# Kernel tuning notes

Hardware: AMD Instinct MI355X
Metric: run time of the kernel (lower is better)

Reference implementation:

```python
import jax, jax.numpy as jnp
import numpy as np

B, SQ, SE, H, NH = 2, 2048, 2048, 1024, 16
HD = H // NH  # 64

def setup_inputs() -> dict:
    key = jax.random.key(0)
    ks = jax.random.split(key, 8)
    s = 1.0 / np.sqrt(H)
    return {
        "hidden_states": jax.random.normal(ks[0], (B, SQ, H), jnp.float32),
        "encoder_hidden_states": jax.random.normal(ks[1], (B, SE, H), jnp.float32),
        "attention_mask": jnp.zeros((B, 1, 1, SQ + SE), jnp.float32),
        "Wq": jax.random.normal(ks[2], (H, H), jnp.float32) * s,
        "bq": jnp.zeros((H,), jnp.float32),
        "Wk": jax.random.normal(ks[3], (H, H), jnp.float32) * s,
        "bk": jnp.zeros((H,), jnp.float32),
        "Wv": jax.random.normal(ks[4], (H, H), jnp.float32) * s,
        "bv": jnp.zeros((H,), jnp.float32),
    }

def _split_heads(x):
    # [B, S, H] -> [B, NH, S, HD]
    b, s, _ = x.shape
    return x.reshape(b, s, NH, HD).transpose(0, 2, 1, 3)

def reference(hidden_states, encoder_hidden_states, attention_mask, Wq, bq, Wk, bk, Wv, bv):
    # Q from self tokens; K,V from concat(self, encoder) along sequence
    all_hs = jnp.concatenate([hidden_states, encoder_hidden_states], axis=1)  # [B, SQ+SE, H]
    q = _split_heads(hidden_states @ Wq + bq)   # [B, NH, SQ, HD]
    k = _split_heads(all_hs @ Wk + bk)          # [B, NH, SKV, HD]
    v = _split_heads(all_hs @ Wv + bv)          # [B, NH, SKV, HD]
    scores = jnp.einsum('bhqd,bhkd->bhqk', q, k) / jnp.sqrt(jnp.float32(HD))
    scores = scores + attention_mask            # additive mask, broadcast [B,1,1,SKV]
    probs = jax.nn.softmax(scores, axis=-1)     # dropout p=0 (eval)
    ctx = jnp.einsum('bhqk,bhkd->bhqd', probs, v)
    ctx = ctx.transpose(0, 2, 1, 3).reshape(hidden_states.shape[0], hidden_states.shape[1], H)
    return ctx
```

## Files before the change

### kernel.cpp

```cpp
#include <hip/hip_runtime.h>
#include <hip/hip_bf16.h>
#include <stdint.h>


typedef __attribute__((ext_vector_type(8))) short short8;
typedef __attribute__((ext_vector_type(4))) float f32x4;
typedef __attribute__((ext_vector_type(16))) float f32x16;
typedef __attribute__((ext_vector_type(4))) unsigned short us4;
typedef __attribute__((ext_vector_type(4))) unsigned int u32x4;

typedef __attribute__((ext_vector_type(8), may_alias)) short short8a;
typedef __attribute__((ext_vector_type(4), may_alias)) float f32x4a;
typedef __attribute__((may_alias)) float floata;

#define DEV static __device__ __forceinline__

DEV unsigned short f2bf(float f) {
  unsigned int u = __builtin_bit_cast(unsigned int, f);
  u += 0x7fffu + ((u >> 16) & 1u);
  return (unsigned short)(u >> 16);
}

DEV float exp2_(float x) {
#if __has_builtin(__builtin_amdgcn_exp2f)
  return __builtin_amdgcn_exp2f(x);
#else
  float r; asm("v_exp_f32 %0, %1" : "=v"(r) : "v"(x)); return r;
#endif
}

DEV unsigned int cvtpk_bf16(float lo, float hi) {
  unsigned int r;
  asm("v_cvt_pk_bf16_f32 %0, %1, %2" : "=v"(r) : "v"(lo), "v"(hi));
  return r;
}

DEV void g2lds16(const void* g, void* l) {
  __builtin_amdgcn_global_load_lds((const __attribute__((address_space(1))) void*)g,
                                   (__attribute__((address_space(3))) void*)l, 16, 0, 0);
}

__global__ __launch_bounds__(256) void convert_allhs(const float* __restrict__ hid,
                                                     const float* __restrict__ enc,
                                                     unsigned short* __restrict__ ah) {
  int idx = blockIdx.x * 256 + threadIdx.x;
  const int perB = 4096 * 256;
  int b = idx / perB, r = idx - b * perB;
  int s = r >> 8, c4 = r & 255;
  const float* srcrow = (s < 2048) ? hid + (size_t)(b * 2048 + s) * 1024
                                   : enc + (size_t)(b * 2048 + (s - 2048)) * 1024;
  f32x4 v = *(const f32x4*)(srcrow + c4 * 4);
  us4 o;
  o[0] = f2bf(v[0]); o[1] = f2bf(v[1]); o[2] = f2bf(v[2]); o[3] = f2bf(v[3]);
  *(us4*)(ah + (size_t)idx * 4) = o;
}

__global__ __launch_bounds__(256) void premul_mask(const float* __restrict__ m,
                                                   float* __restrict__ o) {
  int i = blockIdx.x * 256 + threadIdx.x;
  o[i] = m[i] * 1.4426950408889634f;
}

__global__ __launch_bounds__(256) void transpose_w3(const float* __restrict__ Wq,
                                                    const float* __restrict__ Wk,
                                                    const float* __restrict__ Wv,
                                                    unsigned short* __restrict__ WtBase) {
  __shared__ unsigned short t[64][65];
  const int z = blockIdx.z;
  const float* W = (z == 0) ? Wq : (z == 1) ? Wk : Wv;
  unsigned short* Wt = WtBase + (size_t)z * 1048576;
  int k0 = blockIdx.y * 64, n0 = blockIdx.x * 64;
  int tid = threadIdx.x;
#pragma unroll
  for (int rep = 0; rep < 16; rep++) {
    int idx = rep * 256 + tid;
    int kk = idx >> 6, nn = idx & 63;
    t[kk][nn] = f2bf(W[(size_t)(k0 + kk) * 1024 + n0 + nn]);
  }
  __syncthreads();
#pragma unroll
  for (int rep = 0; rep < 16; rep++) {
    int idx = rep * 256 + tid;
    int nn = idx >> 6, kk = idx & 63;
    Wt[(size_t)(n0 + nn) * 1024 + k0 + kk] = t[kk][nn];
  }
}

__global__ __launch_bounds__(256) void gemm_all(const unsigned short* __restrict__ WTQ,
                                                const unsigned short* __restrict__ WTK,
                                                const unsigned short* __restrict__ WTV,
                                                const unsigned short* __restrict__ AH,
                                                const float* __restrict__ bq,
                                                const float* __restrict__ bk,
                                                const float* __restrict__ bv,
                                                unsigned short* __restrict__ Qout,
                                                unsigned short* __restrict__ Kout,
                                                unsigned short* __restrict__ Vout,
                                                float qscale) {
  __shared__ unsigned short ldsA[128 * 32];
  __shared__ unsigned short ldsB[128 * 32];

  int id = blockIdx.x;
  int f2 = (id & 7) * 160 + (id >> 3);

  const unsigned short *A, *Bm;
  const float* bias;
  unsigned short* outb;
  int S, mode, r0, c0;
  float osc = 1.0f;
  if (f2 < 256) {
    int t = f2;
    int b = t >> 7; t &= 127;
    c0 = (t & 15) * 128; r0 = (t >> 4) * 128;
    A = WTQ; Bm = AH + (size_t)b * 4194304; bias = bq;
    outb = Qout + (size_t)b * 2097152; S = 2048; mode = 0; osc = qscale;
  } else if (f2 < 768) {
    int t = f2 - 256;
    int b = t >> 8; t &= 255;
    c0 = (t & 31) * 128; r0 = (t >> 5) * 128;
    A = WTK; Bm = AH + (size_t)b * 4194304; bias = bk;
    outb = Kout + (size_t)b * 4194304; S = 4096; mode = 0;
  } else {
    int t = f2 - 768;
    int b = t >> 8; t &= 255;
    c0 = (t & 7) * 128; r0 = (t >> 3) * 128;
    A = AH + (size_t)b * 4194304; Bm = WTV; bias = bv;
    outb = Vout + (size_t)b * 4194304; S = 4096; mode = 1;
  }

  const int tid = threadIdx.x, w = tid >> 6, l = tid & 63;
  const int wr = w >> 1, wc = w & 1;
  const int lrow = l >> 2, lk = (l & 3) * 8;
  const int lc = l & 15, g = l >> 4;

  f32x4 acc[4][4];
#pragma unroll
  for (int i = 0; i < 4; i++)
#pragma unroll
    for (int j = 0; j < 4; j++) acc[i][j] = (f32x4){0.f, 0.f, 0.f, 0.f};

  for (int k0 = 0; k0 < 1024; k0 += 32) {
#pragma unroll
    for (int t = 0; t < 2; t++) {
      const int tt = w * 2 + t;
      g2lds16(A + (size_t)(r0 + tt * 16 + lrow) * 1024 + k0 + lk, (char*)ldsA + tt * 1024);
      g2lds16(Bm + (size_t)(c0 + tt * 16 + lrow) * 1024 + k0 + lk, (char*)ldsB + tt * 1024);
    }
    __syncthreads();
    short8 af[4], bf[4];
#pragma unroll
    for (int f = 0; f < 4; f++) {
      af[f] = *(const short8*)((const char*)ldsA + (wr * 64 + f * 16 + lc) * 64 + g * 16);
      bf[f] = *(const short8*)((const char*)ldsB + (wc * 64 + f * 16 + lc) * 64 + g * 16);
    }
#pragma unroll
    for (int fr = 0; fr < 4; fr++)
#pragma unroll
      for (int fc = 0; fc < 4; fc++)
        acc[fr][fc] = __builtin_amdgcn_mfma_f32_16x16x32_bf16(af[fr], bf[fc], acc[fr][fc], 0, 0, 0);
    __syncthreads();
  }

#pragma unroll
  for (int fr = 0; fr < 4; fr++) {
    int rb = r0 + wr * 64 + fr * 16 + g * 4;
    float bv4[4];
    if (mode == 0) {
#pragma unroll
      for (int i = 0; i < 4; i++) bv4[i] = bias[rb + i];
    }
#pragma unroll
    for (int fc = 0; fc < 4; fc++) {
      int c = c0 + wc * 64 + fc * 16 + lc;
      float bc = (mode == 0) ? 0.f : bias[c];
      us4 pk;
#pragma unroll
      for (int i = 0; i < 4; i++) {
        float v = (acc[fr][fc][i] + (mode == 0 ? bv4[i] : bc)) * osc;
        pk[i] = f2bf(v);
      }
      size_t addr;
      if (mode == 0) addr = ((size_t)(rb >> 6) * S + c) * 64 + (rb & 63);
      else           addr = (size_t)c * S + rb;
      *(us4*)(outb + addr) = pk;
    }
  }
}

__global__ __launch_bounds__(256) void attn_kernel(const unsigned short* __restrict__ Q,
                                                   const unsigned short* __restrict__ K,
                                                   const unsigned short* __restrict__ Vt,
                                                   const float* __restrict__ mask2,
                                                   float* __restrict__ out) {
  __shared__ __align__(16) char lds[32768];

  int flat = blockIdx.x + 16 * (blockIdx.y + 16 * blockIdx.z);
  int f2 = (flat & 7) * 64 + (flat >> 3);
  const int qt = f2 & 15, h = (f2 >> 4) & 15, b = f2 >> 8;

  const int tid = threadIdx.x, w = tid >> 6, l = tid & 63;
  const int lq = l & 31, h2 = l >> 5;
  const int isV = w >> 1, half = w & 1;
  const int srow8 = l >> 3, slot = l & 7;

  const unsigned short* Qb = Q + ((size_t)(b * 16 + h) * 2048) * 64;
  const unsigned short* Kb = K + ((size_t)(b * 16 + h) * 4096) * 64;
  const unsigned short* Vb = Vt + ((size_t)(b * 16 + h) * 64) * 4096;
  const float* mk = mask2 + (size_t)b * 4096;
  const int sq0 = qt * 128 + w * 32;

  short8 qf[4];
#pragma unroll
  for (int ks = 0; ks < 4; ks++)
    qf[ks] = *(const short8*)(Qb + (size_t)(sq0 + lq) * 64 + ks * 16 + h2 * 8);

  f32x16 ctx[2];
#pragma unroll
  for (int d = 0; d < 2; d++)
#pragma unroll
    for (int r = 0; r < 16; r++) ctx[d][r] = 0.f;
  float lsr = 0.f;

  {
    char* base = lds + isV * 8192;
    if (!isV) {
#pragma unroll
      for (int c = 0; c < 4; c++) {
        int kr = half * 32 + c * 8 + srow8;
        g2lds16(Kb + (size_t)kr * 64 + (slot ^ (kr & 7)) * 8, base + (half * 32 + c * 8) * 128);
      }
    } else {
#pragma unroll
      for (int c = 0; c < 4; c++) {
        int dr = half * 32 + c * 8 + srow8;
        g2lds16(Vb + (size_t)dr * 4096 + (slot ^ (dr & 7)) * 8, base + (half * 32 + c * 8) * 128);
      }
    }
  }
  __syncthreads();

  int buf = 0;
  for (int t = 0; t < 64; t++) {
    const int s0 = t * 64;

    f32x4 mv[2][4];
#pragma unroll
    for (int sub = 0; sub < 2; sub++)
#pragma unroll
      for (int br = 0; br < 4; br++)
        mv[sub][br] = *(const f32x4*)(mk + s0 + sub * 32 + br * 8 + h2 * 4);

    if (t < 63) {
      char* base = lds + (buf ^ 1) * 16384 + isV * 8192;
      if (!isV) {
#pragma unroll
        for (int c = 0; c < 4; c++) {
          int kr = half * 32 + c * 8 + srow8;
          g2lds16(Kb + (size_t)(s0 + 64 + kr) * 64 + (slot ^ (kr & 7)) * 8,
                  base + (half * 32 + c * 8) * 128);
        }
      } else {
#pragma unroll
        for (int c = 0; c < 4; c++) {
          int dr = half * 32 + c * 8 + srow8;
          g2lds16(Vb + (size_t)dr * 4096 + (s0 + 64) + (slot ^ (dr & 7)) * 8,
                  base + (half * 32 + c * 8) * 128);
        }
      }
    }

    const char* kbase = lds + buf * 16384;
    const char* vbase = lds + buf * 16384 + 8192;

    short8 bfr[2][2];
#pragma unroll
    for (int sub = 0; sub < 2; sub++) {
      f32x16 z;
#pragma unroll
      for (int br = 0; br < 4; br++)
#pragma unroll
        for (int i = 0; i < 4; i++) z[br * 4 + i] = mv[sub][br][i];
#pragma unroll
      for (int ks = 0; ks < 4; ks++) {
        short8 kf = *(const short8*)(kbase + (sub * 32 + lq) * 128 + (((ks * 2 + h2) ^ (lq & 7)) << 4));
        z = __builtin_amdgcn_mfma_f32_32x32x16_bf16(kf, qf[ks], z, 0, 0, 0);
      }
      float p[16];
#pragma unroll
      for (int r = 0; r < 16; r++) { p[r] = exp2_(z[r]); lsr += p[r]; }
      unsigned int X[4], Y[4];
#pragma unroll
      for (int br = 0; br < 4; br++) {
        X[br] = cvtpk_bf16(p[br * 4 + 0], p[br * 4 + 1]);
        Y[br] = cvtpk_bf16(p[br * 4 + 2], p[br * 4 + 3]);
      }
#pragma unroll
      for (int k2 = 0; k2 < 2; k2++) {
        unsigned int xd = X[2 * k2], xs = X[2 * k2 + 1];
        asm("v_permlane32_swap_b32 %0, %1" : "+v"(xd), "+v"(xs));
        unsigned int yd = Y[2 * k2], ys = Y[2 * k2 + 1];
        asm("v_permlane32_swap_b32 %0, %1" : "+v"(yd), "+v"(ys));
        u32x4 packed = (u32x4){xd, yd, xs, ys};
        bfr[sub][k2] = __builtin_bit_cast(short8, packed);
      }
    }

#pragma unroll
    for (int dsub = 0; dsub < 2; dsub++)
#pragma unroll
      for (int sub = 0; sub < 2; sub++)
#pragma unroll
        for (int k2 = 0; k2 < 2; k2++) {
          short8 vf = *(const short8*)(vbase + (dsub * 32 + lq) * 128 +
                                       (((sub * 4 + k2 * 2 + h2) ^ (lq & 7)) << 4));
          ctx[dsub] = __builtin_amdgcn_mfma_f32_32x32x16_bf16(vf, bfr[sub][k2], ctx[dsub], 0, 0, 0);
        }

    __syncthreads();
    buf ^= 1;
  }

  float ls_tot = lsr + __shfl_xor(lsr, 32, 64);
  float inv = 1.f / ls_tot;

  size_t orow = (size_t)(b * 2048 + sq0 + lq);
#pragma unroll
  for (int dsub = 0; dsub < 2; dsub++)
#pragma unroll
    for (int br = 0; br < 4; br++) {
      int d0 = dsub * 32 + br * 8 + h2 * 4;
      f32x4 o = (f32x4){ctx[dsub][br * 4 + 0], ctx[dsub][br * 4 + 1],
                        ctx[dsub][br * 4 + 2], ctx[dsub][br * 4 + 3]} * inv;
      *(f32x4*)(out + orow * 1024 + h * 64 + d0) = o;
    }
}

extern "C" void kernel_launch(void* const* d_in, const int* in_sizes, int n_in,
                              void* d_out, int out_size, void* d_ws, size_t ws_size,
                              hipStream_t stream) {
  const float* hid = (const float*)d_in[0];
  const float* enc = (const float*)d_in[1];
  const float* mask = (const float*)d_in[2];
  const float* Wq = (const float*)d_in[3];
  const float* bq = (const float*)d_in[4];
  const float* Wk = (const float*)d_in[5];
  const float* bk = (const float*)d_in[6];
  const float* Wv = (const float*)d_in[7];
  const float* bv = (const float*)d_in[8];

  unsigned short* ws = (unsigned short*)d_ws;
  unsigned short* WTQ = ws;
  unsigned short* WTK = ws + 1048576;
  unsigned short* WTV = ws + 2097152;
  unsigned short* AH  = ws + 3145728;
  unsigned short* Qb  = ws + 11534336;
  unsigned short* Kb  = ws + 15728640;
  unsigned short* VT  = ws + 24117248;
  float* mask2 = (float*)(ws + 32505856);

  const float QSCALE = 0.18033688011112042f;

  convert_allhs<<<8192, 256, 0, stream>>>(hid, enc, AH);
  premul_mask<<<32, 256, 0, stream>>>(mask, mask2);
  transpose_w3<<<dim3(16, 16, 3), 256, 0, stream>>>(Wq, Wk, Wv, WTQ);

  gemm_all<<<1280, 256, 0, stream>>>(WTQ, WTK, WTV, AH, bq, bk, bv, Qb, Kb, VT, QSCALE);

  attn_kernel<<<dim3(16, 16, 2), 256, 0, stream>>>(Qb, Kb, VT, mask2, (float*)d_out);
}
```

Before: 186.0 us.

## Split attention KV range into two halves and merge partial results

The attention kernel now handles half of the 4096-long KV sequence per block, doubling the grid from 512 to 1024 blocks. Each block writes unnormalized partial context and row sums to workspace. A new merge kernel adds the two halves and divides by the combined sum. The goal is more waves in flight per CU to hide latency, paid for by an extra kernel launch and extra global traffic for the fp32 partials. The merge only adds the halves, so it relies on the softmax not tracking a per-half running max.

```diff
diff --git a/kernel.cpp b/kernel.cpp
--- a/kernel.cpp
+++ b/kernel.cpp
@@ -191,12 +191,13 @@
                                                    const unsigned short* __restrict__ K,
                                                    const unsigned short* __restrict__ Vt,
                                                    const float* __restrict__ mask2,
-                                                   float* __restrict__ out) {
+                                                   float* __restrict__ ctxP,
+                                                   float* __restrict__ lsP) {
   __shared__ __align__(16) char lds[32768];
 
-  int flat = blockIdx.x + 16 * (blockIdx.y + 16 * blockIdx.z);
-  int f2 = (flat & 7) * 64 + (flat >> 3);
-  const int qt = f2 & 15, h = (f2 >> 4) & 15, b = f2 >> 8;
+  int flat = blockIdx.x + 32 * (blockIdx.y + 16 * blockIdx.z);
+  int f2 = (flat & 7) * 128 + (flat >> 3);
+  const int qt = f2 & 15, kvh = (f2 >> 4) & 1, h = (f2 >> 5) & 15, b = f2 >> 9;
 
   const int tid = threadIdx.x, w = tid >> 6, l = tid & 63;
   const int lq = l & 31, h2 = l >> 5;
@@ -204,9 +205,9 @@
   const int srow8 = l >> 3, slot = l & 7;
 
   const unsigned short* Qb = Q + ((size_t)(b * 16 + h) * 2048) * 64;
-  const unsigned short* Kb = K + ((size_t)(b * 16 + h) * 4096) * 64;
-  const unsigned short* Vb = Vt + ((size_t)(b * 16 + h) * 64) * 4096;
-  const float* mk = mask2 + (size_t)b * 4096;
+  const unsigned short* Kb = K + ((size_t)((b * 16 + h) * 4096 + kvh * 2048)) * 64;
+  const unsigned short* Vb = Vt + ((size_t)(b * 16 + h) * 64) * 4096 + kvh * 2048;
+  const float* mk = mask2 + (size_t)b * 4096 + kvh * 2048;
   const int sq0 = qt * 128 + w * 32;
 
   short8 qf[4];
@@ -240,7 +241,7 @@
   __syncthreads();
 
   int buf = 0;
-  for (int t = 0; t < 64; t++) {
+  for (int t = 0; t < 32; t++) {
     const int s0 = t * 64;
 
     f32x4 mv[2][4];
@@ -250,7 +251,7 @@
       for (int br = 0; br < 4; br++)
         mv[sub][br] = *(const f32x4*)(mk + s0 + sub * 32 + br * 8 + h2 * 4);
 
-    if (t < 63) {
+    if (t < 31) {
       char* base = lds + (buf ^ 1) * 16384 + isV * 8192;
       if (!isV) {
 #pragma unroll
@@ -321,18 +322,31 @@
   }
 
   float ls_tot = lsr + __shfl_xor(lsr, 32, 64);
-  float inv = 1.f / ls_tot;
-
-  size_t orow = (size_t)(b * 2048 + sq0 + lq);
+
+  size_t prow = (size_t)(b * 16 + h) * 2048 + sq0 + lq;
+  float* cp = ctxP + (size_t)kvh * 4194304 + prow * 64;
 #pragma unroll
   for (int dsub = 0; dsub < 2; dsub++)
 #pragma unroll
     for (int br = 0; br < 4; br++) {
       int d0 = dsub * 32 + br * 8 + h2 * 4;
-      f32x4 o = (f32x4){ctx[dsub][br * 4 + 0], ctx[dsub][br * 4 + 1],
-                        ctx[dsub][br * 4 + 2], ctx[dsub][br * 4 + 3]} * inv;
-      *(f32x4*)(out + orow * 1024 + h * 64 + d0) = o;
-    }
+      f32x4 v = (f32x4){ctx[dsub][br * 4 + 0], ctx[dsub][br * 4 + 1],
+                        ctx[dsub][br * 4 + 2], ctx[dsub][br * 4 + 3]};
+      *(f32x4*)(cp + d0) = v;
+    }
+  if (h2 == 0) lsP[kvh * 65536 + prow] = ls_tot;
+}
+
+__global__ __launch_bounds__(256) void merge_halves(const float* __restrict__ ctxP,
+                                                    const float* __restrict__ lsP,
+                                                    float* __restrict__ out) {
+  int idx = blockIdx.x * 256 + threadIdx.x;
+  int row = idx >> 4, d4 = idx & 15;
+  f32x4 c0 = *(const f32x4*)(ctxP + (size_t)row * 64 + d4 * 4);
+  f32x4 c1 = *(const f32x4*)(ctxP + 4194304 + (size_t)row * 64 + d4 * 4);
+  float inv = 1.f / (lsP[row] + lsP[65536 + row]);
+  int b = row >> 15, h = (row >> 11) & 15, q = row & 2047;
+  *(f32x4*)(out + ((size_t)(b * 2048 + q)) * 1024 + h * 64 + d4 * 4) = (c0 + c1) * inv;
 }
 
 extern "C" void kernel_launch(void* const* d_in, const int* in_sizes, int n_in,
@@ -357,6 +371,8 @@
   unsigned short* Kb  = ws + 15728640;
   unsigned short* VT  = ws + 24117248;
   float* mask2 = (float*)(ws + 32505856);
+  float* ctxP  = (float*)(ws + 32522240);
+  float* lsP   = (float*)(ws + 49299456);
 
   const float QSCALE = 0.18033688011112042f;
 
@@ -366,5 +382,6 @@
 
   gemm_all<<<1280, 256, 0, stream>>>(WTQ, WTK, WTV, AH, bq, bk, bv, Qb, Kb, VT, QSCALE);
 
-  attn_kernel<<<dim3(16, 16, 2), 256, 0, stream>>>(Qb, Kb, VT, mask2, (float*)d_out);
-}
+  attn_kernel<<<dim3(32, 16, 2), 256, 0, stream>>>(Qb, Kb, VT, mask2, ctxP, lsP);
+  merge_halves<<<4096, 256, 0, stream>>>(ctxP, lsP, (float*)d_out);
+}
```

After: 198.1 us. +6.5%, slower.
